# Performance work log

Hardware: AMD Instinct MI355X
Metric: run time of the kernel (lower is better)

## Reference

```python
import jax, jax.numpy as jnp
import numpy as np

B, N, L, D = 8, 2048, 4, 256


def setup_inputs() -> dict:
    key = jax.random.key(0)
    k1, k2, k3 = jax.random.split(key, 3)
    prop_state = jax.random.normal(k1, (B, N, L, D), dtype=jnp.float32)
    # dense representation of the (batch, n_node, n_node) sparse adjacency
    A = jax.random.uniform(k2, (B, N, N), dtype=jnp.float32)
    # nn.Linear(state_dim, state_dim): weight ~ N(0, 0.02), bias = 0
    W = jax.random.normal(k3, (D, D), dtype=jnp.float32) * 0.02
    b = jnp.zeros((D,), dtype=jnp.float32)
    return {"prop_state": prop_state, "A": A, "W": W, "b": b}


def reference(prop_state, A, W, b):
    # AH[b,n,l,d] = sum_m A[b,n,m] * prop_state[b,m,l,d]
    AH = jnp.einsum('bnm,bmld->bnld', A, prop_state)
    # Linear + ReLU (torch: F.relu(self.gcn_weight(AH)))
    AHW = jnp.einsum('bnld,ed->bnle', AH, W) + b
    return jax.nn.relu(AHW)
```

## Files before the change

kernel.cpp:

```cpp
#include <hip/hip_runtime.h>
#include <hip/hip_bf16.h>
#include <stdint.h>


typedef __bf16 bf16;
typedef __attribute__((ext_vector_type(8))) __bf16 bf16x8;
typedef __attribute__((ext_vector_type(4))) __bf16 bf16x4;
typedef __attribute__((ext_vector_type(4))) float f32x4;

#define B_  8
#define N_  2048
#define L_  4
#define D_  256
#define LD_ 1024
#define BK  64
#define NT  (N_ / BK)
#define NI  (NT / 2)

__device__ __forceinline__ void gl16(const char* g, char* l) {
  __builtin_amdgcn_global_load_lds((const __attribute__((address_space(1))) void*)g,
                                   (__attribute__((address_space(3))) void*)l, 16, 0, 0);
}

__device__ inline void cvt_store8(const float* __restrict__ s, bf16* d) {
  float4 x = ((const float4*)s)[0];
  float4 y = ((const float4*)s)[1];
  bf16x8 o;
  o[0] = (bf16)x.x; o[1] = (bf16)x.y; o[2] = (bf16)x.z; o[3] = (bf16)x.w;
  o[4] = (bf16)y.x; o[5] = (bf16)y.y; o[6] = (bf16)y.z; o[7] = (bf16)y.w;
  *(bf16x8*)d = o;
}

__global__ __launch_bounds__(256) void pre_kernel(const float* __restrict__ H,
                                                  const float* __restrict__ Wm,
                                                  const float* __restrict__ A,
                                                  bf16* __restrict__ outT,
                                                  bf16* __restrict__ a16) {
  __shared__ __attribute__((aligned(16))) bf16 Ah[128 * 64];
  __shared__ __attribute__((aligned(16))) bf16 Wt[128 * 64];

  if (blockIdx.x >= 1024) {
    const int n8 = (int)((size_t)B_ * N_ * N_ / 8);
    int i = (blockIdx.x - 1024) * 256 + threadIdx.x;
    for (; i < n8; i += 2048 * 256) {
      const float4* s = (const float4*)A + (size_t)i * 2;
      float4 x = s[0], y = s[1];
      bf16x8 o;
      o[0] = (bf16)x.x; o[1] = (bf16)x.y; o[2] = (bf16)x.z; o[3] = (bf16)x.w;
      o[4] = (bf16)y.x; o[5] = (bf16)y.y; o[6] = (bf16)y.z; o[7] = (bf16)y.w;
      *(bf16x8*)(a16 + (size_t)i * 8) = o;
    }
    return;
  }

  const int bid = blockIdx.x;
  const int b   = bid >> 7;
  const int rem = bid & 127;
  const int te  = rem & 1;
  const int tr  = rem >> 1;
  const int r0  = tr * 128;
  const int e0  = te * 128;

  const int t    = threadIdx.x;
  const int lane = t & 63;
  const int wave = t >> 6;
  const int wr = wave >> 1, wc = wave & 1;

  const f32x4 zero = {0.f, 0.f, 0.f, 0.f};
  f32x4 acc[4][4];
  for (int m = 0; m < 4; ++m)
    for (int n = 0; n < 4; ++n) acc[m][n] = zero;

  const float* Hb = H + (size_t)b * (N_ * L_ * D_);
  const int mrow = t >> 3;
  const int colb = (t & 7) * 8;

  for (int k0 = 0; k0 < D_; k0 += 64) {
#pragma unroll
    for (int i = 0; i < 4; ++i) {
      const int r_local = mrow * 4 + i;
      cvt_store8(Hb + (size_t)(r0 + r_local) * D_ + k0 + colb,
                 Ah + (size_t)t * 8 + i * 2048);
      const int erow = i * 32 + mrow;
      cvt_store8(Wm + (size_t)(e0 + erow) * D_ + k0 + colb,
                 Wt + (size_t)t * 8 + i * 2048);
    }
    __syncthreads();
#pragma unroll
    for (int kk = 0; kk < 2; ++kk) {
      bf16x8 af[4], bg[4];
#pragma unroll
      for (int m = 0; m < 4; ++m)
        af[m] = *(const bf16x8*)&Ah[(wr * 64 + m * 16 + (lane & 15)) * 64 + kk * 32 + (lane >> 4) * 8];
#pragma unroll
      for (int n = 0; n < 4; ++n)
        bg[n] = *(const bf16x8*)&Wt[(wc * 64 + n * 16 + (lane & 15)) * 64 + kk * 32 + (lane >> 4) * 8];
#pragma unroll
      for (int m = 0; m < 4; ++m)
#pragma unroll
        for (int n = 0; n < 4; ++n)
          acc[m][n] = __builtin_amdgcn_mfma_f32_16x16x32_bf16(af[m], bg[n], acc[m][n], 0, 0, 0);
    }
    __syncthreads();
  }

  bf16* ob = outT + (size_t)b * (LD_ * N_);
  const int m0 = tr * 32;
#pragma unroll
  for (int m16 = 0; m16 < 4; ++m16) {
    const int qrow = wr * 64 + m16 * 16 + ((lane >> 4) << 2);
    const int l  = qrow >> 5;
    const int ml = qrow & 31;
#pragma unroll
    for (int n = 0; n < 4; ++n) {
      const int e = e0 + wc * 64 + n * 16 + (lane & 15);
      bf16x4 v;
      v[0] = (bf16)acc[m16][n][0]; v[1] = (bf16)acc[m16][n][1];
      v[2] = (bf16)acc[m16][n][2]; v[3] = (bf16)acc[m16][n][3];
      *(bf16x4*)&ob[(size_t)(l * 256 + e) * N_ + m0 + ml] = v;
    }
  }
}

__global__ __launch_bounds__(512, 2) void gemm8p_kernel(
    const bf16* __restrict__ A16, const bf16* __restrict__ HWT,
    const float* __restrict__ bias, float* __restrict__ out) {

  __shared__ __attribute__((aligned(128))) char smem[131072];

  const int bid = blockIdx.x;
  const int lg  = (bid & 7) * 32 + (bid >> 3);
  const int b   = lg >> 5;
  const int tn  = (lg >> 2) & 7;
  const int tc  = lg & 3;
  const int n0  = tn * 256;
  const int c0  = tc * 256;

  const int t    = threadIdx.x;
  const int lane = t & 63;
  const int w    = t >> 6;
  const int wm   = w >> 2;
  const int wn   = w & 3;
  const int l15  = lane & 15;
  const int cg   = lane >> 4;
  const int sl0  = cg ^ (lane & 7);

  const char* Ab = (const char*)(A16 + (size_t)b * N_ * N_);
  const char* Hb = (const char*)(HWT + (size_t)b * LD_ * N_);
  const int  grow  = t >> 3;
  const int  gslot = ((t & 7) ^ (grow & 7)) << 4;
  const char* pA = Ab + (size_t)(n0 + grow) * (N_ * 2) + gslot;
  const char* pB = Hb + (size_t)(c0 + grow) * (N_ * 2) + gslot;
  char* lbase = (char*)smem + t * 16;

#define STAGE(buf, isB, half, kt) do {                                        \
    const char* gp_ = ((isB) ? pB : pA) + (size_t)((half) * 128) * (N_ * 2)   \
                      + (size_t)(kt) * (BK * 2);                              \
    char* lp_ = lbase + (buf) * 65536 + (isB) * 32768 + (half) * 16384;       \
    gl16(gp_, lp_);                                                           \
    gl16(gp_ + (size_t)64 * (N_ * 2), lp_ + 8192);                            \
  } while (0)

#define LDA(buf, mh, fm, kk)                                                  \
  (*(const bf16x8*)(smem + (buf) * 65536 +                                    \
      (wm * 128 + (mh) * 64 + (fm) * 16 + l15) * 128 +                        \
      ((sl0 ^ ((kk) * 4)) << 4)))

#define LDB(buf, fn, kk)                                                      \
  (*(const bf16x8*)(smem + (buf) * 65536 + 32768 +                            \
      (wn * 64 + (fn) * 16 + l15) * 128 +                                     \
      ((sl0 ^ ((kk) * 4)) << 4)))

#define MFMA16(base, AF, BF)                                                  \
  do {                                                                        \
    __builtin_amdgcn_s_setprio(1);                                            \
    _Pragma("unroll")                                                         \
    for (int fm_ = 0; fm_ < 4; ++fm_)                                         \
      _Pragma("unroll")                                                       \
      for (int fn_ = 0; fn_ < 4; ++fn_)                                       \
        acc[(base) + fm_][fn_] = __builtin_amdgcn_mfma_f32_16x16x32_bf16(     \
            AF[fm_], BF[fn_], acc[(base) + fm_][fn_], 0, 0, 0);               \
    __builtin_amdgcn_s_setprio(0);                                            \
  } while (0)

#define BARRIER() do { __builtin_amdgcn_s_barrier();                          \
                       asm volatile("" ::: "memory"); } while (0)
#define VMCNT0_BAR() do {                                                     \
    asm volatile("s_waitcnt vmcnt(0)" ::: "memory");                          \
    __builtin_amdgcn_sched_barrier(0);                                        \
    BARRIER(); } while (0)

  f32x4 acc[8][4];
#pragma unroll
  for (int i_ = 0; i_ < 8; ++i_)
#pragma unroll
    for (int j_ = 0; j_ < 4; ++j_) acc[i_][j_] = (f32x4){0.f, 0.f, 0.f, 0.f};

  bf16x8 aX[4], aY[4], bA[4], bB[4];

  STAGE(0, 0, 0, 0); STAGE(0, 0, 1, 0); STAGE(0, 1, 0, 0); STAGE(0, 1, 1, 0);
  VMCNT0_BAR();
#pragma unroll
  for (int fm = 0; fm < 4; ++fm) aY[fm] = LDA(0, 0, fm, 0);
#pragma unroll
  for (int fn = 0; fn < 4; ++fn) bA[fn] = LDB(0, fn, 0);

#pragma unroll 1
  for (int i = 0; i < NI; ++i) {
    const int kt1 = 2 * i + 1;
    const int kt2 = (2 * i + 2 < NT) ? 2 * i + 2 : NT - 2;

#pragma unroll
    for (int fm = 0; fm < 4; ++fm) aX[fm] = LDA(0, 0, fm, 1);
#pragma unroll
    for (int fn = 0; fn < 4; ++fn) bB[fn] = LDB(0, fn, 1);
    STAGE(1, 0, 0, kt1); STAGE(1, 0, 1, kt1); STAGE(1, 1, 0, kt1);
    MFMA16(0, aY, bA);

#pragma unroll
    for (int fm = 0; fm < 4; ++fm) aY[fm] = LDA(0, 1, fm, 0);
    STAGE(1, 1, 1, kt1);
    MFMA16(0, aX, bB);

#pragma unroll
    for (int fm = 0; fm < 4; ++fm) aX[fm] = LDA(0, 1, fm, 1);
    MFMA16(4, aY, bA);
    VMCNT0_BAR();

#pragma unroll
    for (int fm = 0; fm < 4; ++fm) aY[fm] = LDA(1, 0, fm, 0);
#pragma unroll
    for (int fn = 0; fn < 4; ++fn) bA[fn] = LDB(1, fn, 0);
    MFMA16(4, aX, bB);
    BARRIER();

#pragma unroll
    for (int fm = 0; fm < 4; ++fm) aX[fm] = LDA(1, 0, fm, 1);
#pragma unroll
    for (int fn = 0; fn < 4; ++fn) bB[fn] = LDB(1, fn, 1);
    STAGE(0, 0, 0, kt2); STAGE(0, 0, 1, kt2); STAGE(0, 1, 0, kt2);
    MFMA16(0, aY, bA);

#pragma unroll
    for (int fm = 0; fm < 4; ++fm) aY[fm] = LDA(1, 1, fm, 0);
    STAGE(0, 1, 1, kt2);
    MFMA16(0, aX, bB);

#pragma unroll
    for (int fm = 0; fm < 4; ++fm) aX[fm] = LDA(1, 1, fm, 1);
    MFMA16(4, aY, bA);
    VMCNT0_BAR();

#pragma unroll
    for (int fm = 0; fm < 4; ++fm) aY[fm] = LDA(0, 0, fm, 0);
#pragma unroll
    for (int fn = 0; fn < 4; ++fn) bA[fn] = LDB(0, fn, 0);
    MFMA16(4, aX, bB);
    BARRIER();
  }

  float* ob = out + (size_t)b * N_ * LD_;
  const int orow0 = n0 + wm * 128 + cg * 4;
  const int ocol0 = c0 + wn * 64 + l15;
#pragma unroll
  for (int mh = 0; mh < 2; ++mh)
#pragma unroll
    for (int fm = 0; fm < 4; ++fm) {
      const int r = orow0 + mh * 64 + fm * 16;
#pragma unroll
      for (int fn = 0; fn < 4; ++fn) {
        const int c = ocol0 + fn * 16;
        const float bv = bias[c & 255];
        const f32x4 v = acc[mh * 4 + fm][fn];
#pragma unroll
        for (int j = 0; j < 4; ++j) {
          const float x = v[j] + bv;
          ob[(size_t)(r + j) * LD_ + c] = x > 0.f ? x : 0.f;
        }
      }
    }
#undef STAGE
#undef LDA
#undef LDB
#undef MFMA16
#undef BARRIER
#undef VMCNT0_BAR
}

extern "C" void kernel_launch(void* const* d_in, const int* in_sizes, int n_in,
                              void* d_out, int out_size, void* d_ws, size_t ws_size,
                              hipStream_t stream) {
  const float* H    = (const float*)d_in[0];
  const float* A    = (const float*)d_in[1];
  const float* Wm   = (const float*)d_in[2];
  const float* bias = (const float*)d_in[3];
  float* out = (float*)d_out;

  const size_t hwt_bytes = (size_t)B_ * LD_ * N_ * sizeof(bf16);
  const size_t a16_bytes = (size_t)B_ * N_ * N_ * sizeof(bf16);
  if (ws_size < hwt_bytes + a16_bytes) return;

  bf16* hwt = (bf16*)d_ws;
  bf16* a16 = (bf16*)((char*)d_ws + hwt_bytes);

  pre_kernel<<<dim3(3072), dim3(256), 0, stream>>>(H, Wm, A, hwt, a16);
  gemm8p_kernel<<<dim3(256), dim3(512), 0, stream>>>(a16, hwt, bias, out);
}
```

Baseline: 132.1 us.

## Fuse fp32-to-bf16 conversion of adjacency into GEMM A-tile loading

Removes the separate pass that converts A (128MB fp32) to a bf16 workspace. The GEMM now loads fp32 A tiles through registers, converts them, and writes them to LDS, while H·W^T tiles still arrive by direct global-to-LDS loads. The M tile shrinks from 256 to 128 rows, doubling the grid to 512 blocks and cutting LDS to 96KB. This saves a 128MB read plus a 64MB write and read round trip. In exchange it adds register-staged loads, VALU conversion in the main loop, and more re-reads of the B operand because the tiles are smaller.

```diff
diff --git a/kernel.cpp b/kernel.cpp
--- a/kernel.cpp
+++ b/kernel.cpp
@@ -31,28 +31,9 @@
   *(bf16x8*)d = o;
 }
 
-__global__ __launch_bounds__(256) void pre_kernel(const float* __restrict__ H,
+__global__ __launch_bounds__(256) void hwt_kernel(const float* __restrict__ H,
                                                   const float* __restrict__ Wm,
-                                                  const float* __restrict__ A,
-                                                  bf16* __restrict__ outT,
-                                                  bf16* __restrict__ a16) {
-  __shared__ __attribute__((aligned(16))) bf16 Ah[128 * 64];
-  __shared__ __attribute__((aligned(16))) bf16 Wt[128 * 64];
-
-  if (blockIdx.x >= 1024) {
-    const int n8 = (int)((size_t)B_ * N_ * N_ / 8);
-    int i = (blockIdx.x - 1024) * 256 + threadIdx.x;
-    for (; i < n8; i += 2048 * 256) {
-      const float4* s = (const float4*)A + (size_t)i * 2;
-      float4 x = s[0], y = s[1];
-      bf16x8 o;
-      o[0] = (bf16)x.x; o[1] = (bf16)x.y; o[2] = (bf16)x.z; o[3] = (bf16)x.w;
-      o[4] = (bf16)y.x; o[5] = (bf16)y.y; o[6] = (bf16)y.z; o[7] = (bf16)y.w;
-      *(bf16x8*)(a16 + (size_t)i * 8) = o;
-    }
-    return;
-  }
-
+                                                  bf16* __restrict__ outT) {
   const int bid = blockIdx.x;
   const int b   = bid >> 7;
   const int rem = bid & 127;
@@ -60,6 +41,9 @@
   const int tr  = rem >> 1;
   const int r0  = tr * 128;
   const int e0  = te * 128;
+
+  __shared__ __attribute__((aligned(16))) bf16 Ah[128 * 64];
+  __shared__ __attribute__((aligned(16))) bf16 Wt[128 * 64];
 
   const int t    = threadIdx.x;
   const int lane = t & 63;
@@ -122,18 +106,18 @@
   }
 }
 
-__global__ __launch_bounds__(512, 2) void gemm8p_kernel(
-    const bf16* __restrict__ A16, const bf16* __restrict__ HWT,
+__global__ __launch_bounds__(512, 2) void gemm_fp32a_kernel(
+    const float* __restrict__ Af, const bf16* __restrict__ HWT,
     const float* __restrict__ bias, float* __restrict__ out) {
 
-  __shared__ __attribute__((aligned(128))) char smem[131072];
+  __shared__ __attribute__((aligned(128))) char smem[98304];
 
   const int bid = blockIdx.x;
-  const int lg  = (bid & 7) * 32 + (bid >> 3);
-  const int b   = lg >> 5;
-  const int tn  = (lg >> 2) & 7;
+  const int lg  = (bid & 7) * 64 + (bid >> 3);
+  const int b   = lg >> 6;
+  const int tn  = (lg >> 2) & 15;
   const int tc  = lg & 3;
-  const int n0  = tn * 256;
+  const int n0  = tn * 128;
   const int c0  = tc * 256;
 
   const int t    = threadIdx.x;
@@ -145,63 +129,89 @@
   const int cg   = lane >> 4;
   const int sl0  = cg ^ (lane & 7);
 
-  const char* Ab = (const char*)(A16 + (size_t)b * N_ * N_);
   const char* Hb = (const char*)(HWT + (size_t)b * LD_ * N_);
-  const int  grow  = t >> 3;
-  const int  gslot = ((t & 7) ^ (grow & 7)) << 4;
-  const char* pA = Ab + (size_t)(n0 + grow) * (N_ * 2) + gslot;
+  const int grow  = t >> 3;
+  const int gslot = ((t & 7) ^ (grow & 7)) << 4;
   const char* pB = Hb + (size_t)(c0 + grow) * (N_ * 2) + gslot;
-  char* lbase = (char*)smem + t * 16;
-
-#define STAGE(buf, isB, half, kt) do {                                        \
-    const char* gp_ = ((isB) ? pB : pA) + (size_t)((half) * 128) * (N_ * 2)   \
+  char* lB = (char*)smem + 16384 + t * 16;
+
+  const float* Ab = Af + (size_t)b * N_ * N_;
+  const int rA = t >> 2;
+  const int cq = t & 3;
+  const float* pA = Ab + (size_t)(n0 + rA) * N_ + cq * 16;
+  char* wA0 = (char*)smem + rA * 128 + ((((2 * cq)     ^ (rA & 7))) << 4);
+  char* wA1 = (char*)smem + rA * 128 + ((((2 * cq + 1) ^ (rA & 7))) << 4);
+
+  float4 av0, av1, av2, av3;
+
+#define ALOAD(kt) do {                                                        \
+    const float4* ap_ = (const float4*)(pA + (size_t)(kt) * BK);              \
+    av0 = ap_[0]; av1 = ap_[1]; av2 = ap_[2]; av3 = ap_[3];                   \
+  } while (0)
+
+#define AWRITE(buf) do {                                                      \
+    bf16x8 o0_, o1_;                                                          \
+    o0_[0]=(bf16)av0.x; o0_[1]=(bf16)av0.y; o0_[2]=(bf16)av0.z;               \
+    o0_[3]=(bf16)av0.w; o0_[4]=(bf16)av1.x; o0_[5]=(bf16)av1.y;               \
+    o0_[6]=(bf16)av1.z; o0_[7]=(bf16)av1.w;                                   \
+    o1_[0]=(bf16)av2.x; o1_[1]=(bf16)av2.y; o1_[2]=(bf16)av2.z;               \
+    o1_[3]=(bf16)av2.w; o1_[4]=(bf16)av3.x; o1_[5]=(bf16)av3.y;               \
+    o1_[6]=(bf16)av3.z; o1_[7]=(bf16)av3.w;                                   \
+    *(bf16x8*)(wA0 + (buf) * 49152) = o0_;                                    \
+    *(bf16x8*)(wA1 + (buf) * 49152) = o1_;                                    \
+  } while (0)
+
+#define STAGEB(buf, half, kt) do {                                            \
+    const char* gp_ = pB + (size_t)((half) * 128) * (N_ * 2)                  \
                       + (size_t)(kt) * (BK * 2);                              \
-    char* lp_ = lbase + (buf) * 65536 + (isB) * 32768 + (half) * 16384;       \
+    char* lp_ = lB + (buf) * 49152 + (half) * 16384;                          \
     gl16(gp_, lp_);                                                           \
     gl16(gp_ + (size_t)64 * (N_ * 2), lp_ + 8192);                            \
   } while (0)
 
-#define LDA(buf, mh, fm, kk)                                                  \
-  (*(const bf16x8*)(smem + (buf) * 65536 +                                    \
-      (wm * 128 + (mh) * 64 + (fm) * 16 + l15) * 128 +                        \
-      ((sl0 ^ ((kk) * 4)) << 4)))
+#define LDA(buf, fm, kk)                                                      \
+  (*(const bf16x8*)(smem + (buf) * 49152 +                                    \
+      (wm * 64 + (fm) * 16 + l15) * 128 + ((sl0 ^ ((kk) * 4)) << 4)))
 
 #define LDB(buf, fn, kk)                                                      \
-  (*(const bf16x8*)(smem + (buf) * 65536 + 32768 +                            \
-      (wn * 64 + (fn) * 16 + l15) * 128 +                                     \
-      ((sl0 ^ ((kk) * 4)) << 4)))
-
-#define MFMA16(base, AF, BF)                                                  \
+  (*(const bf16x8*)(smem + (buf) * 49152 + 16384 +                            \
+      (wn * 64 + (fn) * 16 + l15) * 128 + ((sl0 ^ ((kk) * 4)) << 4)))
+
+#define MFMA8(fh, AF, BF)                                                     \
   do {                                                                        \
     __builtin_amdgcn_s_setprio(1);                                            \
     _Pragma("unroll")                                                         \
-    for (int fm_ = 0; fm_ < 4; ++fm_)                                         \
+    for (int fm_ = 0; fm_ < 2; ++fm_)                                         \
       _Pragma("unroll")                                                       \
       for (int fn_ = 0; fn_ < 4; ++fn_)                                       \
-        acc[(base) + fm_][fn_] = __builtin_amdgcn_mfma_f32_16x16x32_bf16(     \
-            AF[fm_], BF[fn_], acc[(base) + fm_][fn_], 0, 0, 0);               \
+        acc[(fh) * 2 + fm_][fn_] = __builtin_amdgcn_mfma_f32_16x16x32_bf16(   \
+            AF[fm_], BF[fn_], acc[(fh) * 2 + fm_][fn_], 0, 0, 0);             \
     __builtin_amdgcn_s_setprio(0);                                            \
   } while (0)
 
 #define BARRIER() do { __builtin_amdgcn_s_barrier();                          \
                        asm volatile("" ::: "memory"); } while (0)
-#define VMCNT0_BAR() do {                                                     \
-    asm volatile("s_waitcnt vmcnt(0)" ::: "memory");                          \
+#define READY_BAR() do {                                                      \
+    asm volatile("s_waitcnt vmcnt(0) lgkmcnt(0)" ::: "memory");               \
     __builtin_amdgcn_sched_barrier(0);                                        \
     BARRIER(); } while (0)
-
-  f32x4 acc[8][4];
-#pragma unroll
-  for (int i_ = 0; i_ < 8; ++i_)
+#define VM4() asm volatile("s_waitcnt vmcnt(4)" ::: "memory")
+
+  f32x4 acc[4][4];
+#pragma unroll
+  for (int i_ = 0; i_ < 4; ++i_)
 #pragma unroll
     for (int j_ = 0; j_ < 4; ++j_) acc[i_][j_] = (f32x4){0.f, 0.f, 0.f, 0.f};
 
-  bf16x8 aX[4], aY[4], bA[4], bB[4];
-
-  STAGE(0, 0, 0, 0); STAGE(0, 0, 1, 0); STAGE(0, 1, 0, 0); STAGE(0, 1, 1, 0);
-  VMCNT0_BAR();
-#pragma unroll
-  for (int fm = 0; fm < 4; ++fm) aY[fm] = LDA(0, 0, fm, 0);
+  bf16x8 aX[2], aY[2], bA[4], bB[4];
+
+  ALOAD(0);
+  STAGEB(0, 0, 0); STAGEB(0, 1, 0);
+  VM4();
+  AWRITE(0);
+  READY_BAR();
+#pragma unroll
+  for (int fm = 0; fm < 2; ++fm) aY[fm] = LDA(0, fm, 0);
 #pragma unroll
   for (int fn = 0; fn < 4; ++fn) bA[fn] = LDB(0, fn, 0);
 
@@ -211,80 +221,87 @@
     const int kt2 = (2 * i + 2 < NT) ? 2 * i + 2 : NT - 2;
 
 #pragma unroll
-    for (int fm = 0; fm < 4; ++fm) aX[fm] = LDA(0, 0, fm, 1);
+    for (int fm = 0; fm < 2; ++fm) aX[fm] = LDA(0, fm, 1);
 #pragma unroll
     for (int fn = 0; fn < 4; ++fn) bB[fn] = LDB(0, fn, 1);
-    STAGE(1, 0, 0, kt1); STAGE(1, 0, 1, kt1); STAGE(1, 1, 0, kt1);
-    MFMA16(0, aY, bA);
-
-#pragma unroll
-    for (int fm = 0; fm < 4; ++fm) aY[fm] = LDA(0, 1, fm, 0);
-    STAGE(1, 1, 1, kt1);
-    MFMA16(0, aX, bB);
-
-#pragma unroll
-    for (int fm = 0; fm < 4; ++fm) aX[fm] = LDA(0, 1, fm, 1);
-    MFMA16(4, aY, bA);
-    VMCNT0_BAR();
-
-#pragma unroll
-    for (int fm = 0; fm < 4; ++fm) aY[fm] = LDA(1, 0, fm, 0);
+    ALOAD(kt1);
+    STAGEB(1, 0, kt1);
+    MFMA8(0, aY, bA);
+
+#pragma unroll
+    for (int fm = 0; fm < 2; ++fm) aY[fm] = LDA(0, 2 + fm, 0);
+    STAGEB(1, 1, kt1);
+    VM4();
+    AWRITE(1);
+    MFMA8(0, aX, bB);
+
+#pragma unroll
+    for (int fm = 0; fm < 2; ++fm) aX[fm] = LDA(0, 2 + fm, 1);
+    MFMA8(1, aY, bA);
+    READY_BAR();
+
+#pragma unroll
+    for (int fm = 0; fm < 2; ++fm) aY[fm] = LDA(1, fm, 0);
 #pragma unroll
     for (int fn = 0; fn < 4; ++fn) bA[fn] = LDB(1, fn, 0);
-    MFMA16(4, aX, bB);
+    MFMA8(1, aX, bB);
     BARRIER();
 
 #pragma unroll
-    for (int fm = 0; fm < 4; ++fm) aX[fm] = LDA(1, 0, fm, 1);
+    for (int fm = 0; fm < 2; ++fm) aX[fm] = LDA(1, fm, 1);
 #pragma unroll
     for (int fn = 0; fn < 4; ++fn) bB[fn] = LDB(1, fn, 1);
-    STAGE(0, 0, 0, kt2); STAGE(0, 0, 1, kt2); STAGE(0, 1, 0, kt2);
-    MFMA16(0, aY, bA);
-
-#pragma unroll
-    for (int fm = 0; fm < 4; ++fm) aY[fm] = LDA(1, 1, fm, 0);
-    STAGE(0, 1, 1, kt2);
-    MFMA16(0, aX, bB);
-
-#pragma unroll
-    for (int fm = 0; fm < 4; ++fm) aX[fm] = LDA(1, 1, fm, 1);
-    MFMA16(4, aY, bA);
-    VMCNT0_BAR();
-
-#pragma unroll
-    for (int fm = 0; fm < 4; ++fm) aY[fm] = LDA(0, 0, fm, 0);
+    ALOAD(kt2);
+    STAGEB(0, 0, kt2);
+    MFMA8(0, aY, bA);
+
+#pragma unroll
+    for (int fm = 0; fm < 2; ++fm) aY[fm] = LDA(1, 2 + fm, 0);
+    STAGEB(0, 1, kt2);
+    VM4();
+    AWRITE(0);
+    MFMA8(0, aX, bB);
+
+#pragma unroll
+    for (int fm = 0; fm < 2; ++fm) aX[fm] = LDA(1, 2 + fm, 1);
+    MFMA8(1, aY, bA);
+    READY_BAR();
+
+#pragma unroll
+    for (int fm = 0; fm < 2; ++fm) aY[fm] = LDA(0, fm, 0);
 #pragma unroll
     for (int fn = 0; fn < 4; ++fn) bA[fn] = LDB(0, fn, 0);
-    MFMA16(4, aX, bB);
+    MFMA8(1, aX, bB);
     BARRIER();
   }
 
   float* ob = out + (size_t)b * N_ * LD_;
-  const int orow0 = n0 + wm * 128 + cg * 4;
+  const int orow0 = n0 + wm * 64 + cg * 4;
   const int ocol0 = c0 + wn * 64 + l15;
 #pragma unroll
-  for (int mh = 0; mh < 2; ++mh)
-#pragma unroll
-    for (int fm = 0; fm < 4; ++fm) {
-      const int r = orow0 + mh * 64 + fm * 16;
-#pragma unroll
-      for (int fn = 0; fn < 4; ++fn) {
-        const int c = ocol0 + fn * 16;
-        const float bv = bias[c & 255];
-        const f32x4 v = acc[mh * 4 + fm][fn];
-#pragma unroll
-        for (int j = 0; j < 4; ++j) {
-          const float x = v[j] + bv;
-          ob[(size_t)(r + j) * LD_ + c] = x > 0.f ? x : 0.f;
-        }
+  for (int fm = 0; fm < 4; ++fm) {
+    const int r = orow0 + fm * 16;
+#pragma unroll
+    for (int fn = 0; fn < 4; ++fn) {
+      const int c = ocol0 + fn * 16;
+      const float bv = bias[c & 255];
+      const f32x4 v = acc[fm][fn];
+#pragma unroll
+      for (int j = 0; j < 4; ++j) {
+        const float x = v[j] + bv;
+        ob[(size_t)(r + j) * LD_ + c] = x > 0.f ? x : 0.f;
       }
     }
-#undef STAGE
+  }
+#undef ALOAD
+#undef AWRITE
+#undef STAGEB
 #undef LDA
 #undef LDB
-#undef MFMA16
+#undef MFMA8
 #undef BARRIER
-#undef VMCNT0_BAR
+#undef READY_BAR
+#undef VM4
 }
 
 extern "C" void kernel_launch(void* const* d_in, const int* in_sizes, int n_in,
@@ -297,12 +314,10 @@
   float* out = (float*)d_out;
 
   const size_t hwt_bytes = (size_t)B_ * LD_ * N_ * sizeof(bf16);
-  const size_t a16_bytes = (size_t)B_ * N_ * N_ * sizeof(bf16);
-  if (ws_size < hwt_bytes + a16_bytes) return;
+  if (ws_size < hwt_bytes) return;
 
   bf16* hwt = (bf16*)d_ws;
-  bf16* a16 = (bf16*)((char*)d_ws + hwt_bytes);
-
-  pre_kernel<<<dim3(3072), dim3(256), 0, stream>>>(H, Wm, A, hwt, a16);
-  gemm8p_kernel<<<dim3(256), dim3(512), 0, stream>>>(a16, hwt, bias, out);
-}
+
+  hwt_kernel<<<dim3(1024), dim3(256), 0, stream>>>(H, Wm, hwt);
+  gemm_fp32a_kernel<<<dim3(512), dim3(512), 0, stream>>>(A, hwt, bias, out);
+}
```

After: 196.2 us. 48.5% more time.

## Split A conversion into its own kernel and swizzle LDS in H·W^T GEMM

Applied to the files above, without the earlier changes.

Splits the combined pre-kernel into a standalone fp32→bf16 conversion kernel for A and a separate H·W^T GEMM kernel. The GEMM kernel now stores bf16 tiles in LDS with an XOR swizzle on 16-byte chunks, meant to remove bank conflicts on the MFMA operand reads. The split lets each kernel use its own resources and drops the branch inside one kernel. The cost is one extra kernel launch, and the two pre-stages no longer overlap inside a single grid.

```diff
diff --git a/kernel.cpp b/kernel.cpp
--- a/kernel.cpp
+++ b/kernel.cpp
@@ -22,37 +22,27 @@
                                    (__attribute__((address_space(3))) void*)l, 16, 0, 0);
 }
 
-__device__ inline void cvt_store8(const float* __restrict__ s, bf16* d) {
+__device__ inline void cvt8(const float* __restrict__ s, bf16x8* o) {
   float4 x = ((const float4*)s)[0];
   float4 y = ((const float4*)s)[1];
-  bf16x8 o;
-  o[0] = (bf16)x.x; o[1] = (bf16)x.y; o[2] = (bf16)x.z; o[3] = (bf16)x.w;
-  o[4] = (bf16)y.x; o[5] = (bf16)y.y; o[6] = (bf16)y.z; o[7] = (bf16)y.w;
-  *(bf16x8*)d = o;
-}
-
-__global__ __launch_bounds__(256) void pre_kernel(const float* __restrict__ H,
+  (*o)[0] = (bf16)x.x; (*o)[1] = (bf16)x.y; (*o)[2] = (bf16)x.z; (*o)[3] = (bf16)x.w;
+  (*o)[4] = (bf16)y.x; (*o)[5] = (bf16)y.y; (*o)[6] = (bf16)y.z; (*o)[7] = (bf16)y.w;
+}
+
+__global__ __launch_bounds__(256) void cvt_a_kernel(const float* __restrict__ src,
+                                                    bf16* __restrict__ dst, int n8) {
+  int i = blockIdx.x * 256 + threadIdx.x;
+  const int stride = gridDim.x * 256;
+  for (; i < n8; i += stride) {
+    bf16x8 o;
+    cvt8(src + (size_t)i * 8, &o);
+    *(bf16x8*)(dst + (size_t)i * 8) = o;
+  }
+}
+
+__global__ __launch_bounds__(256) void hwt_kernel(const float* __restrict__ H,
                                                   const float* __restrict__ Wm,
-                                                  const float* __restrict__ A,
-                                                  bf16* __restrict__ outT,
-                                                  bf16* __restrict__ a16) {
-  __shared__ __attribute__((aligned(16))) bf16 Ah[128 * 64];
-  __shared__ __attribute__((aligned(16))) bf16 Wt[128 * 64];
-
-  if (blockIdx.x >= 1024) {
-    const int n8 = (int)((size_t)B_ * N_ * N_ / 8);
-    int i = (blockIdx.x - 1024) * 256 + threadIdx.x;
-    for (; i < n8; i += 2048 * 256) {
-      const float4* s = (const float4*)A + (size_t)i * 2;
-      float4 x = s[0], y = s[1];
-      bf16x8 o;
-      o[0] = (bf16)x.x; o[1] = (bf16)x.y; o[2] = (bf16)x.z; o[3] = (bf16)x.w;
-      o[4] = (bf16)y.x; o[5] = (bf16)y.y; o[6] = (bf16)y.z; o[7] = (bf16)y.w;
-      *(bf16x8*)(a16 + (size_t)i * 8) = o;
-    }
-    return;
-  }
-
+                                                  bf16* __restrict__ outT) {
   const int bid = blockIdx.x;
   const int b   = bid >> 7;
   const int rem = bid & 127;
@@ -61,10 +51,15 @@
   const int r0  = tr * 128;
   const int e0  = te * 128;
 
+  __shared__ __attribute__((aligned(16))) char Ah[128 * 128];
+  __shared__ __attribute__((aligned(16))) char Wt[128 * 128];
+
   const int t    = threadIdx.x;
   const int lane = t & 63;
   const int wave = t >> 6;
   const int wr = wave >> 1, wc = wave & 1;
+  const int l15 = lane & 15;
+  const int cg  = lane >> 4;
 
   const f32x4 zero = {0.f, 0.f, 0.f, 0.f};
   f32x4 acc[4][4];
@@ -74,27 +69,33 @@
   const float* Hb = H + (size_t)b * (N_ * L_ * D_);
   const int mrow = t >> 3;
   const int colb = (t & 7) * 8;
+  const int woff = (t >> 3) * 128 + (((t & 7) ^ ((t >> 3) & 7)) << 4);
 
   for (int k0 = 0; k0 < D_; k0 += 64) {
 #pragma unroll
     for (int i = 0; i < 4; ++i) {
       const int r_local = mrow * 4 + i;
-      cvt_store8(Hb + (size_t)(r0 + r_local) * D_ + k0 + colb,
-                 Ah + (size_t)t * 8 + i * 2048);
+      bf16x8 oa, ow;
+      cvt8(Hb + (size_t)(r0 + r_local) * D_ + k0 + colb, &oa);
       const int erow = i * 32 + mrow;
-      cvt_store8(Wm + (size_t)(e0 + erow) * D_ + k0 + colb,
-                 Wt + (size_t)t * 8 + i * 2048);
+      cvt8(Wm + (size_t)(e0 + erow) * D_ + k0 + colb, &ow);
+      *(bf16x8*)(Ah + woff + i * 4096) = oa;
+      *(bf16x8*)(Wt + woff + i * 4096) = ow;
     }
     __syncthreads();
 #pragma unroll
     for (int kk = 0; kk < 2; ++kk) {
       bf16x8 af[4], bg[4];
 #pragma unroll
-      for (int m = 0; m < 4; ++m)
-        af[m] = *(const bf16x8*)&Ah[(wr * 64 + m * 16 + (lane & 15)) * 64 + kk * 32 + (lane >> 4) * 8];
-#pragma unroll
-      for (int n = 0; n < 4; ++n)
-        bg[n] = *(const bf16x8*)&Wt[(wc * 64 + n * 16 + (lane & 15)) * 64 + kk * 32 + (lane >> 4) * 8];
+      for (int m = 0; m < 4; ++m) {
+        const int row = wr * 64 + m * 16 + l15;
+        af[m] = *(const bf16x8*)&Ah[row * 128 + (((kk * 4 + cg) ^ (row & 7)) << 4)];
+      }
+#pragma unroll
+      for (int n = 0; n < 4; ++n) {
+        const int row = wc * 64 + n * 16 + l15;
+        bg[n] = *(const bf16x8*)&Wt[row * 128 + (((kk * 4 + cg) ^ (row & 7)) << 4)];
+      }
 #pragma unroll
       for (int m = 0; m < 4; ++m)
 #pragma unroll
@@ -108,12 +109,12 @@
   const int m0 = tr * 32;
 #pragma unroll
   for (int m16 = 0; m16 < 4; ++m16) {
-    const int qrow = wr * 64 + m16 * 16 + ((lane >> 4) << 2);
+    const int qrow = wr * 64 + m16 * 16 + (cg << 2);
     const int l  = qrow >> 5;
     const int ml = qrow & 31;
 #pragma unroll
     for (int n = 0; n < 4; ++n) {
-      const int e = e0 + wc * 64 + n * 16 + (lane & 15);
+      const int e = e0 + wc * 64 + n * 16 + l15;
       bf16x4 v;
       v[0] = (bf16)acc[m16][n][0]; v[1] = (bf16)acc[m16][n][1];
       v[2] = (bf16)acc[m16][n][2]; v[3] = (bf16)acc[m16][n][3];
@@ -303,6 +304,8 @@
   bf16* hwt = (bf16*)d_ws;
   bf16* a16 = (bf16*)((char*)d_ws + hwt_bytes);
 
-  pre_kernel<<<dim3(3072), dim3(256), 0, stream>>>(H, Wm, A, hwt, a16);
+  cvt_a_kernel<<<dim3(2048), dim3(256), 0, stream>>>(A, a16,
+      (int)((size_t)B_ * N_ * N_ / 8));
+  hwt_kernel<<<dim3(1024), dim3(256), 0, stream>>>(H, Wm, hwt);
   gemm8p_kernel<<<dim3(256), dim3(512), 0, stream>>>(a16, hwt, bias, out);
 }
```

After: 135.4 us. 2.5% more time.
